# Performance work log

Measured on AMD Instinct MI355X. Metric: run time of the kernel, lower is better.

The kernel has to match this reference:

```python
import jax, jax.numpy as jnp
import numpy as np

N = 8192
F_IN = 256
F_OUT = 256


def setup_inputs() -> dict:
    key = jax.random.key(0)
    k1, k2, k3, k4 = jax.random.split(key, 4)
    return {
        "input": jax.random.normal(k1, (N, F_IN), dtype=jnp.float32),
        "adj": jax.random.uniform(k2, (N, N), dtype=jnp.float32),
        "weight": jax.random.normal(k3, (F_IN, F_OUT), dtype=jnp.float32) * (1.0 / np.sqrt(F_OUT)),
        "bias": jax.random.normal(k4, (F_OUT,), dtype=jnp.float32) * (1.0 / np.sqrt(F_OUT)),
    }


def reference(input, adj, weight, bias):
    n = input.shape[0]
    # add_identity=True: adj <- adj + I
    a = adj + jnp.eye(n, dtype=adj.dtype)
    # D^{-1/2} as a vector; diag-matmul == row/col elementwise scaling
    d = jax.lax.rsqrt(jnp.sum(a, axis=1))  # [n]
    adj_norm = d[:, None] * a * d[None, :]  # [n, n]
    support = input @ weight                # [n, f_out]
    out = adj_norm @ support + bias         # [n, f_out]
    return out
```

## Files before the change

### kernel.cpp

```cpp
#include <hip/hip_runtime.h>
#include <stdint.h>

#define N_ROWS 8192
#define F_DIM 256
#define SPLITK 4
#define KSTRIP (N_ROWS / SPLITK)

typedef __attribute__((ext_vector_type(8))) short s16x8;
typedef __attribute__((ext_vector_type(4))) short s16x4;
typedef __attribute__((ext_vector_type(4))) float f32x4;
typedef __attribute__((address_space(3))) uint32_t lds_u32_t;
typedef __attribute__((address_space(1))) const uint32_t gbl_u32_t;

__device__ __forceinline__ void gl_lds16(const void* g, void* l) {
    __builtin_amdgcn_global_load_lds((gbl_u32_t*)g, (lds_u32_t*)l, 16, 0, 0);
}

__device__ __forceinline__ unsigned short f2bf(float f) {
    unsigned int u = __float_as_uint(f);
    u += 0x7FFFu + ((u >> 16) & 1u);
    return (unsigned short)(u >> 16);
}
__device__ __forceinline__ float bf2f(unsigned short h) {
    return __uint_as_float(((unsigned int)h) << 16);
}
__device__ __forceinline__ s16x8 cvt8(f32x4 a, f32x4 b) {
    s16x8 r;
    r[0] = (short)f2bf(a[0]); r[1] = (short)f2bf(a[1]);
    r[2] = (short)f2bf(a[2]); r[3] = (short)f2bf(a[3]);
    r[4] = (short)f2bf(b[0]); r[5] = (short)f2bf(b[1]);
    r[6] = (short)f2bf(b[2]); r[7] = (short)f2bf(b[3]);
    return r;
}

__global__ void k_rowsum(const float* __restrict__ adj, float* __restrict__ dvec) {
    const int row = blockIdx.x;
    const float4* p = (const float4*)(adj + (size_t)row * N_ROWS);
    float s = 0.f;
#pragma unroll
    for (int i = 0; i < 8; ++i) {
        float4 v = p[threadIdx.x + i * 256];
        s += (v.x + v.y) + (v.z + v.w);
    }
#pragma unroll
    for (int off = 32; off > 0; off >>= 1) s += __shfl_down(s, off, 64);
    __shared__ float red[4];
    if ((threadIdx.x & 63) == 0) red[threadIdx.x >> 6] = s;
    __syncthreads();
    if (threadIdx.x == 0) {
        float t = red[0] + red[1] + red[2] + red[3] + 1.0f;
        dvec[row] = rsqrtf(t);
    }
}

__global__ void k_wt(const float* __restrict__ w, unsigned short* __restrict__ wt) {
    const int j = blockIdx.x, t = threadIdx.x;
    wt[j * F_DIM + t] = f2bf(w[t * F_DIM + j]);
}

__global__ __launch_bounds__(256, 2)
void k_support(const float* __restrict__ input, const unsigned short* __restrict__ wt,
               const float* __restrict__ dvec, unsigned short* __restrict__ sup,
               unsigned short* __restrict__ sup_t) {
    __shared__ float As[128 * 32];
    __shared__ unsigned short Bs[128 * 32];
    const int tid = threadIdx.x, lane = tid & 63, wid = tid >> 6;
    const int wm = wid & 1, wn = wid >> 1;
    const int l15 = lane & 15, q4 = lane >> 4;
    const int m0 = blockIdx.x * 128, n0 = blockIdx.y * 128;

    uint32_t aoff[4], alds[4], boff[2], blds[2];
#pragma unroll
    for (int i = 0; i < 4; ++i) {
        int row = wid * 32 + i * 8 + (lane >> 3);
        int cg = (lane & 7) ^ (lane >> 3);
        aoff[i] = (uint32_t)(m0 + row) * F_DIM + cg * 4;
        alds[i] = (uint32_t)(wid * 32 + i * 8) * 32;
    }
#pragma unroll
    for (int i = 0; i < 2; ++i) {
        int row = wid * 32 + i * 16 + (lane >> 2);
        int cg = (lane & 3) ^ ((lane >> 3) & 3);
        boff[i] = (uint32_t)(n0 + row) * F_DIM + cg * 8;
        blds[i] = (uint32_t)(wid * 32 + i * 16) * 32;
    }

    const int ra7 = l15 & 7;
    const int rb3 = (l15 >> 1) & 3;
    const f32x4* aptr[4][2];
    const s16x8* bptr[4];
#pragma unroll
    for (int a = 0; a < 4; ++a)
#pragma unroll
        for (int j = 0; j < 2; ++j)
            aptr[a][j] = (const f32x4*)(As + (wm * 64 + a * 16 + l15) * 32
                                        + (((2 * q4 + j) ^ ra7) * 4));
#pragma unroll
    for (int b = 0; b < 4; ++b)
        bptr[b] = (const s16x8*)(Bs + (wn * 64 + b * 16 + l15) * 32 + ((q4 ^ rb3) * 8));

    f32x4 acc[4][4];
#pragma unroll
    for (int a = 0; a < 4; ++a)
#pragma unroll
        for (int b = 0; b < 4; ++b) acc[a][b] = (f32x4){0.f, 0.f, 0.f, 0.f};

#pragma unroll 1
    for (int it = 0; it < F_DIM / 32; ++it) {
        __syncthreads();
#pragma unroll
        for (int i = 0; i < 4; ++i) gl_lds16(input + aoff[i], As + alds[i]);
#pragma unroll
        for (int i = 0; i < 2; ++i) gl_lds16(wt + boff[i], Bs + blds[i]);
        __syncthreads();
        s16x8 af[4];
#pragma unroll
        for (int a = 0; a < 4; ++a) af[a] = cvt8(aptr[a][0][0], aptr[a][1][0]);
#pragma unroll
        for (int b = 0; b < 4; ++b) {
            s16x8 bf = *bptr[b];
#pragma unroll
            for (int a = 0; a < 4; ++a)
                acc[a][b] = __builtin_amdgcn_mfma_f32_16x16x32_bf16(af[a], bf, acc[a][b], 0, 0, 0);
        }
#pragma unroll
        for (int i = 0; i < 4; ++i) aoff[i] += 32;
#pragma unroll
        for (int i = 0; i < 2; ++i) boff[i] += 32;
    }

#pragma unroll
    for (int a = 0; a < 4; ++a) {
        const int rbase = m0 + wm * 64 + a * 16 + q4 * 4;
        float dv[4];
#pragma unroll
        for (int r = 0; r < 4; ++r) dv[r] = dvec[rbase + r];
#pragma unroll
        for (int b = 0; b < 4; ++b) {
            const int col = n0 + wn * 64 + b * 16 + l15;
            f32x4 c = acc[a][b];
            s16x4 pk;
#pragma unroll
            for (int r = 0; r < 4; ++r) {
                unsigned short h = f2bf(dv[r] * c[r]);
                pk[r] = (short)h;
                sup[(size_t)(rbase + r) * F_DIM + col] = h;
            }
            *(s16x4*)(sup_t + (size_t)col * N_ROWS + rbase) = pk;
        }
    }
}

__global__ __launch_bounds__(256, 2)
void k_main(const float* __restrict__ adj, const unsigned short* __restrict__ sup_t,
            float* __restrict__ part) {
    __shared__ float As[64 * 32];
    __shared__ unsigned short Bs[256 * 32];
    const int tid = threadIdx.x, lane = tid & 63, wid = tid >> 6;
    const int l15 = lane & 15, q4 = lane >> 4;
    const int m0 = blockIdx.x * 64;
    const int kbase = blockIdx.y * KSTRIP;

    uint32_t aoff[2], alds[2];
#pragma unroll
    for (int r = 0; r < 2; ++r) {
        int idx = r * 256 + tid;
        int row = idx >> 3;
        int cg = (idx & 7) ^ (row & 7);
        aoff[r] = (uint32_t)(m0 + row) * N_ROWS + kbase + cg * 4;
        alds[r] = (uint32_t)(r * 1024 + wid * 256);
    }
    uint32_t boff[4], blds[4];
#pragma unroll
    for (int r = 0; r < 4; ++r) {
        int idx = r * 256 + tid;
        int row = idx >> 2;
        int cg = (idx & 3) ^ ((row >> 1) & 3);
        boff[r] = (uint32_t)row * N_ROWS + kbase + cg * 8;
        blds[r] = (uint32_t)(r * 2048 + wid * 512);
    }

    const int ra7 = l15 & 7;
    const int rb3 = (l15 >> 1) & 3;
    const f32x4* aptr[4][2];
    const s16x8* bptr[4];
#pragma unroll
    for (int a = 0; a < 4; ++a)
#pragma unroll
        for (int j = 0; j < 2; ++j)
            aptr[a][j] = (const f32x4*)(As + (a * 16 + l15) * 32 + (((2 * q4 + j) ^ ra7) * 4));
#pragma unroll
    for (int b = 0; b < 4; ++b)
        bptr[b] = (const s16x8*)(Bs + (wid * 64 + b * 16 + l15) * 32 + ((q4 ^ rb3) * 8));

    f32x4 acc[4][4];
#pragma unroll
    for (int a = 0; a < 4; ++a)
#pragma unroll
        for (int b = 0; b < 4; ++b) acc[a][b] = (f32x4){0.f, 0.f, 0.f, 0.f};

#pragma unroll 1
    for (int it = 0; it < KSTRIP / 32; ++it) {
        __syncthreads();
#pragma unroll
        for (int r = 0; r < 2; ++r) gl_lds16(adj + aoff[r], As + alds[r]);
#pragma unroll
        for (int r = 0; r < 4; ++r) gl_lds16(sup_t + boff[r], Bs + blds[r]);
        __syncthreads();
        s16x8 af[4];
#pragma unroll
        for (int a = 0; a < 4; ++a) af[a] = cvt8(aptr[a][0][0], aptr[a][1][0]);
#pragma unroll
        for (int b = 0; b < 4; ++b) {
            s16x8 bf = *bptr[b];
#pragma unroll
            for (int a = 0; a < 4; ++a)
                acc[a][b] = __builtin_amdgcn_mfma_f32_16x16x32_bf16(af[a], bf, acc[a][b], 0, 0, 0);
        }
#pragma unroll
        for (int r = 0; r < 2; ++r) aoff[r] += 32;
#pragma unroll
        for (int r = 0; r < 4; ++r) boff[r] += 32;
    }

    float* p = part + (size_t)blockIdx.y * ((size_t)N_ROWS * F_DIM);
#pragma unroll
    for (int a = 0; a < 4; ++a) {
        const int rbase = m0 + a * 16 + q4 * 4;
#pragma unroll
        for (int b = 0; b < 4; ++b) {
            const int col = wid * 64 + b * 16 + l15;
            f32x4 c = acc[a][b];
#pragma unroll
            for (int r = 0; r < 4; ++r)
                p[(size_t)(rbase + r) * F_DIM + col] = c[r];
        }
    }
}

__global__ void k_reduce(const float* __restrict__ part, const unsigned short* __restrict__ sup,
                         const float* __restrict__ dvec, const float* __restrict__ bias,
                         float* __restrict__ out) {
    const int gid = blockIdx.x * 256 + threadIdx.x;
    const int row = gid >> 6;
    const int c = (gid & 63) * 4;
    const size_t off = (size_t)row * F_DIM + c;
    const size_t PS = (size_t)N_ROWS * F_DIM;
    f32x4 v = *(const f32x4*)(part + off);
#pragma unroll
    for (int s = 1; s < SPLITK; ++s) v += *(const f32x4*)(part + s * PS + off);
    const float d = dvec[row];
    const unsigned short* sp = sup + off;
    const f32x4 bb = *(const f32x4*)(bias + c);
    f32x4 o;
#pragma unroll
    for (int r = 0; r < 4; ++r) o[r] = d * (v[r] + bf2f(sp[r])) + bb[r];
    *(f32x4*)(out + off) = o;
}

extern "C" void kernel_launch(void* const* d_in, const int* in_sizes, int n_in,
                              void* d_out, int out_size, void* d_ws, size_t ws_size,
                              hipStream_t stream) {
    const float* input  = (const float*)d_in[0];
    const float* adj    = (const float*)d_in[1];
    const float* weight = (const float*)d_in[2];
    const float* bias   = (const float*)d_in[3];
    float* out = (float*)d_out;

    char* ws = (char*)d_ws;
    float* dvec           = (float*)ws;
    unsigned short* wt    = (unsigned short*)(ws + (32 << 10));
    unsigned short* sup   = (unsigned short*)(ws + (32 << 10) + (128 << 10));
    unsigned short* sup_t = (unsigned short*)(ws + (32 << 10) + (128 << 10)
                                              + (size_t)N_ROWS * F_DIM * 2);
    float* part           = (float*)(ws + (32 << 10) + (128 << 10)
                                     + 2 * (size_t)N_ROWS * F_DIM * 2);

    k_rowsum<<<dim3(N_ROWS), dim3(256), 0, stream>>>(adj, dvec);
    k_wt<<<dim3(F_DIM), dim3(F_DIM), 0, stream>>>(weight, wt);
    k_support<<<dim3(64, 2), dim3(256), 0, stream>>>(input, wt, dvec, sup, sup_t);
    k_main<<<dim3(128, SPLITK), dim3(256), 0, stream>>>(adj, sup_t, part);
    k_reduce<<<dim3((N_ROWS * F_DIM / 4) / 256), dim3(256), 0, stream>>>(part, sup, dvec, bias, out);
}
```

Before: 483.3 us.

## Pre-convert adjacency to bf16 in rowsum pass and double K tile in main GEMM

The row-sum kernel now also writes a bf16 copy of the adjacency matrix while it already streams it. The main split-K GEMM then reads that bf16 copy directly into LDS instead of fp32, so it no longer converts on the fly, and it processes K in tiles of 64 instead of 32. The goal is to roughly halve the bytes the GEMM reads for the adjacency operand and halve the number of barrier-separated iterations. The cost is an extra 128 MB write in the row-sum pass, a larger workspace, and more LDS per block, which could reduce occupancy.

```diff
diff --git a/kernel.cpp b/kernel.cpp
--- a/kernel.cpp
+++ b/kernel.cpp
@@ -5,6 +5,7 @@
 #define F_DIM 256
 #define SPLITK 4
 #define KSTRIP (N_ROWS / SPLITK)
+#define BK 64
 
 typedef __attribute__((ext_vector_type(8))) short s16x8;
 typedef __attribute__((ext_vector_type(4))) short s16x4;
@@ -33,14 +34,20 @@
     return r;
 }
 
-__global__ void k_rowsum(const float* __restrict__ adj, float* __restrict__ dvec) {
+__global__ void k_rowsum(const float* __restrict__ adj, float* __restrict__ dvec,
+                         unsigned short* __restrict__ adj_bf) {
     const int row = blockIdx.x;
     const float4* p = (const float4*)(adj + (size_t)row * N_ROWS);
+    s16x4* q = (s16x4*)(adj_bf + (size_t)row * N_ROWS);
     float s = 0.f;
 #pragma unroll
     for (int i = 0; i < 8; ++i) {
         float4 v = p[threadIdx.x + i * 256];
         s += (v.x + v.y) + (v.z + v.w);
+        s16x4 pk;
+        pk[0] = (short)f2bf(v.x); pk[1] = (short)f2bf(v.y);
+        pk[2] = (short)f2bf(v.z); pk[3] = (short)f2bf(v.w);
+        q[threadIdx.x + i * 256] = pk;
     }
 #pragma unroll
     for (int off = 32; off > 0; off >>= 1) s += __shfl_down(s, off, 64);
@@ -152,10 +159,10 @@
 }
 
 __global__ __launch_bounds__(256, 2)
-void k_main(const float* __restrict__ adj, const unsigned short* __restrict__ sup_t,
+void k_main(const unsigned short* __restrict__ adj_bf, const unsigned short* __restrict__ sup_t,
             float* __restrict__ part) {
-    __shared__ float As[64 * 32];
-    __shared__ unsigned short Bs[256 * 32];
+    __shared__ unsigned short As[64 * 64];
+    __shared__ unsigned short Bs[256 * 64];
     const int tid = threadIdx.x, lane = tid & 63, wid = tid >> 6;
     const int l15 = lane & 15, q4 = lane >> 4;
     const int m0 = blockIdx.x * 64;
@@ -167,31 +174,33 @@
         int idx = r * 256 + tid;
         int row = idx >> 3;
         int cg = (idx & 7) ^ (row & 7);
-        aoff[r] = (uint32_t)(m0 + row) * N_ROWS + kbase + cg * 4;
-        alds[r] = (uint32_t)(r * 1024 + wid * 256);
-    }
-    uint32_t boff[4], blds[4];
-#pragma unroll
-    for (int r = 0; r < 4; ++r) {
+        aoff[r] = (uint32_t)(m0 + row) * N_ROWS + kbase + cg * 8;
+        alds[r] = (uint32_t)(r * 2048 + wid * 512);
+    }
+    uint32_t boff[8], blds[8];
+#pragma unroll
+    for (int r = 0; r < 8; ++r) {
         int idx = r * 256 + tid;
-        int row = idx >> 2;
-        int cg = (idx & 3) ^ ((row >> 1) & 3);
+        int row = idx >> 3;
+        int cg = (idx & 7) ^ (row & 7);
         boff[r] = (uint32_t)row * N_ROWS + kbase + cg * 8;
         blds[r] = (uint32_t)(r * 2048 + wid * 512);
     }
 
     const int ra7 = l15 & 7;
-    const int rb3 = (l15 >> 1) & 3;
-    const f32x4* aptr[4][2];
-    const s16x8* bptr[4];
-#pragma unroll
-    for (int a = 0; a < 4; ++a)
-#pragma unroll
-        for (int j = 0; j < 2; ++j)
-            aptr[a][j] = (const f32x4*)(As + (a * 16 + l15) * 32 + (((2 * q4 + j) ^ ra7) * 4));
+    const s16x8* aptr[4][2];
+    const s16x8* bptr[4][2];
+#pragma unroll
+    for (int a = 0; a < 4; ++a)
+#pragma unroll
+        for (int h = 0; h < 2; ++h)
+            aptr[a][h] = (const s16x8*)(As + (a * 16 + l15) * 64 + (((h * 4 + q4) ^ ra7) * 8));
 #pragma unroll
     for (int b = 0; b < 4; ++b)
-        bptr[b] = (const s16x8*)(Bs + (wid * 64 + b * 16 + l15) * 32 + ((q4 ^ rb3) * 8));
+#pragma unroll
+        for (int h = 0; h < 2; ++h)
+            bptr[b][h] = (const s16x8*)(Bs + (wid * 64 + b * 16 + l15) * 64
+                                        + (((h * 4 + q4) ^ ra7) * 8));
 
     f32x4 acc[4][4];
 #pragma unroll
@@ -200,27 +209,30 @@
         for (int b = 0; b < 4; ++b) acc[a][b] = (f32x4){0.f, 0.f, 0.f, 0.f};
 
 #pragma unroll 1
-    for (int it = 0; it < KSTRIP / 32; ++it) {
-        __syncthreads();
-#pragma unroll
-        for (int r = 0; r < 2; ++r) gl_lds16(adj + aoff[r], As + alds[r]);
-#pragma unroll
-        for (int r = 0; r < 4; ++r) gl_lds16(sup_t + boff[r], Bs + blds[r]);
-        __syncthreads();
-        s16x8 af[4];
-#pragma unroll
-        for (int a = 0; a < 4; ++a) af[a] = cvt8(aptr[a][0][0], aptr[a][1][0]);
-#pragma unroll
-        for (int b = 0; b < 4; ++b) {
-            s16x8 bf = *bptr[b];
-#pragma unroll
-            for (int a = 0; a < 4; ++a)
-                acc[a][b] = __builtin_amdgcn_mfma_f32_16x16x32_bf16(af[a], bf, acc[a][b], 0, 0, 0);
-        }
-#pragma unroll
-        for (int r = 0; r < 2; ++r) aoff[r] += 32;
-#pragma unroll
-        for (int r = 0; r < 4; ++r) boff[r] += 32;
+    for (int it = 0; it < KSTRIP / BK; ++it) {
+        __syncthreads();
+#pragma unroll
+        for (int r = 0; r < 2; ++r) gl_lds16(adj_bf + aoff[r], As + alds[r]);
+#pragma unroll
+        for (int r = 0; r < 8; ++r) gl_lds16(sup_t + boff[r], Bs + blds[r]);
+        __syncthreads();
+#pragma unroll
+        for (int h = 0; h < 2; ++h) {
+            s16x8 af[4];
+#pragma unroll
+            for (int a = 0; a < 4; ++a) af[a] = *aptr[a][h];
+#pragma unroll
+            for (int b = 0; b < 4; ++b) {
+                s16x8 bf = *bptr[b][h];
+#pragma unroll
+                for (int a = 0; a < 4; ++a)
+                    acc[a][b] = __builtin_amdgcn_mfma_f32_16x16x32_bf16(af[a], bf, acc[a][b], 0, 0, 0);
+            }
+        }
+#pragma unroll
+        for (int r = 0; r < 2; ++r) aoff[r] += BK;
+#pragma unroll
+        for (int r = 0; r < 8; ++r) boff[r] += BK;
     }
 
     float* p = part + (size_t)blockIdx.y * ((size_t)N_ROWS * F_DIM);
@@ -268,17 +280,19 @@
     float* out = (float*)d_out;
 
     char* ws = (char*)d_ws;
-    float* dvec           = (float*)ws;
-    unsigned short* wt    = (unsigned short*)(ws + (32 << 10));
-    unsigned short* sup   = (unsigned short*)(ws + (32 << 10) + (128 << 10));
-    unsigned short* sup_t = (unsigned short*)(ws + (32 << 10) + (128 << 10)
+    unsigned short* adj_bf = (unsigned short*)ws;
+    char* ws2 = ws + (size_t)N_ROWS * N_ROWS * 2;
+    float* dvec           = (float*)ws2;
+    unsigned short* wt    = (unsigned short*)(ws2 + (32 << 10));
+    unsigned short* sup   = (unsigned short*)(ws2 + (32 << 10) + (128 << 10));
+    unsigned short* sup_t = (unsigned short*)(ws2 + (32 << 10) + (128 << 10)
                                               + (size_t)N_ROWS * F_DIM * 2);
-    float* part           = (float*)(ws + (32 << 10) + (128 << 10)
+    float* part           = (float*)(ws2 + (32 << 10) + (128 << 10)
                                      + 2 * (size_t)N_ROWS * F_DIM * 2);
 
-    k_rowsum<<<dim3(N_ROWS), dim3(256), 0, stream>>>(adj, dvec);
+    k_rowsum<<<dim3(N_ROWS), dim3(256), 0, stream>>>(adj, dvec, adj_bf);
     k_wt<<<dim3(F_DIM), dim3(F_DIM), 0, stream>>>(weight, wt);
     k_support<<<dim3(64, 2), dim3(256), 0, stream>>>(input, wt, dvec, sup, sup_t);
-    k_main<<<dim3(128, SPLITK), dim3(256), 0, stream>>>(adj, sup_t, part);
+    k_main<<<dim3(128, SPLITK), dim3(256), 0, stream>>>(adj_bf, sup_t, part);
     k_reduce<<<dim3((N_ROWS * F_DIM / 4) / 256), dim3(256), 0, stream>>>(part, sup, dvec, bias, out);
 }
```

Result: faster. 468.6 us (-3.1%).
